# Performance work log

Measured on AMD Instinct MI355X. Metric: run time of the kernel, lower is better.

Reference implementation:

```python
import jax, jax.numpy as jnp
import numpy as np

EMB = 512
HEADS = 8
HEAD_DIM = EMB // HEADS


def setup_inputs() -> dict:
    key = jax.random.key(0)
    ks = jax.random.split(key, 9)
    s = 1.0 / np.sqrt(EMB)
    return {
        "x": jax.random.normal(ks[0], (4, 2048, EMB), dtype=jnp.float32),
        "Wq": jax.random.uniform(ks[1], (EMB, EMB), jnp.float32, -s, s),
        "bq": jax.random.uniform(ks[2], (EMB,), jnp.float32, -s, s),
        "Wk": jax.random.uniform(ks[3], (EMB, EMB), jnp.float32, -s, s),
        "bk": jax.random.uniform(ks[4], (EMB,), jnp.float32, -s, s),
        "Wv": jax.random.uniform(ks[5], (EMB, EMB), jnp.float32, -s, s),
        "bv": jax.random.uniform(ks[6], (EMB,), jnp.float32, -s, s),
        "Wp": jax.random.uniform(ks[7], (EMB, EMB), jnp.float32, -s, s),
        "bp": jax.random.uniform(ks[8], (EMB,), jnp.float32, -s, s),
    }


def _split_heads(t):
    b, n, _ = t.shape
    return t.reshape(b, n, HEADS, HEAD_DIM).transpose(0, 2, 1, 3)  # b h n d


def reference(x, Wq, bq, Wk, bk, Wv, bv, Wp, bp):
    q = _split_heads(x @ Wq.T + bq)
    k = _split_heads(x @ Wk.T + bk)
    v = _split_heads(x @ Wv.T + bv)
    energy = jnp.einsum("bhqd,bhkd->bhqk", q, k)
    # NOTE: original applies softmax to UNSCALED logits, then divides probs by sqrt(emb)
    att = jax.nn.softmax(energy, axis=-1) / jnp.sqrt(jnp.float32(EMB))
    out = jnp.einsum("bhqk,bhkd->bhqd", att, v)
    b, h, n, d = out.shape
    out = out.transpose(0, 2, 1, 3).reshape(b, n, h * d)
    return out @ Wp.T + bp
```

## Files before the change

kernel.cpp:

```cpp
#include <hip/hip_runtime.h>
#include <math.h>
#include <stdint.h>

#define SEQ  2048
#define NH   8
#define HD   64
#define MTOT 8192
#define LOG2E 1.4426950408889634f

typedef __attribute__((ext_vector_type(4))) float f32x4;
typedef __attribute__((ext_vector_type(8))) short bf16x8;

__device__ __forceinline__ unsigned short bfu(float f) {
    return (unsigned short)((__float_as_uint(f) + 0x8000u) >> 16);
}
__device__ __forceinline__ unsigned packbf(float a, float b) {
    return __builtin_amdgcn_perm(__float_as_uint(b) + 0x8000u,
                                 __float_as_uint(a) + 0x8000u, 0x07060302u);
}

__device__ __forceinline__ void gl_lds16(const void* g, const void* l) {
    __builtin_amdgcn_global_load_lds(
        (const __attribute__((address_space(1))) unsigned int*)g,
        (__attribute__((address_space(3))) unsigned int*)l, 16, 0, 0);
}

__global__ __launch_bounds__(256) void convert_kernel(
    const float* __restrict__ x,  const float* __restrict__ wq,
    const float* __restrict__ wk, const float* __restrict__ wv,
    const float* __restrict__ wp, unsigned short* __restrict__ dst)
{
    const long i = ((long)blockIdx.x * 256 + threadIdx.x) * 4;
    if (i >= 5242880L) return;
    const float* src; long off;
    if      (i < 4194304L) { src = x;  off = i; }
    else if (i < 4456448L) { src = wq; off = i - 4194304L; }
    else if (i < 4718592L) { src = wk; off = i - 4456448L; }
    else if (i < 4980736L) { src = wv; off = i - 4718592L; }
    else                   { src = wp; off = i - 4980736L; }
    const float4 a = *(const float4*)(src + off);
    uint2 o;
    o.x = packbf(a.x, a.y);
    o.y = packbf(a.z, a.w);
    *(uint2*)(dst + i) = o;
}

template <int MODE>
__global__ __launch_bounds__(256, 2) void gemm_kernel(
    const unsigned short* __restrict__ A, const unsigned short* __restrict__ W,
    const float* __restrict__ b0, const float* __restrict__ b1,
    const float* __restrict__ b2,
    unsigned short* __restrict__ Qw, unsigned short* __restrict__ Kw,
    unsigned short* __restrict__ VTw, float* __restrict__ Fout)
{
    constexpr int BN = (MODE == 0) ? 128 : 64;
    constexpr int NT = BN / 32;
    constexpr int BSTR = BN * 32;
    __shared__ __align__(16) unsigned short smem[16384];
    const int t = threadIdx.x;
    const int w = t >> 6, lane = t & 63, quad = (t >> 4) & 3, l15 = t & 15;
    const int wr = w >> 1, wc = w & 1;
    const int m0 = blockIdx.y * 128, n0 = blockIdx.x * BN;

    f32x4 acc[4][NT];
#pragma unroll
    for (int mt = 0; mt < 4; ++mt)
#pragma unroll
        for (int nt = 0; nt < NT; ++nt) acc[mt][nt] = (f32x4){0.f, 0.f, 0.f, 0.f};

    auto stage = [&](int buf, int k0) {
#pragma unroll
        for (int i = 0; i < 2; ++i) {
            const int ci = w * 2 + i;
            gl_lds16(A + (size_t)(m0 + ci * 16 + l15) * 512 + k0 + quad * 8,
                     smem + buf * 4096 + ci * 512);
            if (MODE == 0)
                gl_lds16(W + (size_t)(n0 + ci * 16 + l15) * 512 + k0 + quad * 8,
                         smem + 8192 + buf * BSTR + ci * 512);
        }
        if (MODE == 1)
            gl_lds16(W + (size_t)(n0 + w * 16 + l15) * 512 + k0 + quad * 8,
                     smem + 8192 + buf * BSTR + w * 512);
    };

    stage(0, 0);
    __syncthreads();
    int buf = 0;
    for (int ki = 0; ki < 16; ++ki) {
        if (ki < 15) stage(buf ^ 1, (ki + 1) * 32);
        const unsigned short* As = smem + buf * 4096;
        const unsigned short* Bs = smem + 8192 + buf * BSTR;
        bf16x8 af[4], bfr[NT];
#pragma unroll
        for (int mt = 0; mt < 4; ++mt)
            af[mt] = *(const bf16x8*)(As + ((wr * 4 + mt) * 64 + lane) * 8);
#pragma unroll
        for (int nt = 0; nt < NT; ++nt)
            bfr[nt] = *(const bf16x8*)(Bs + ((wc * NT + nt) * 64 + lane) * 8);
#pragma unroll
        for (int mt = 0; mt < 4; ++mt)
#pragma unroll
            for (int nt = 0; nt < NT; ++nt)
                acc[mt][nt] = __builtin_amdgcn_mfma_f32_16x16x32_bf16(
                    af[mt], bfr[nt], acc[mt][nt], 0, 0, 0);
        buf ^= 1;
        if (ki < 15) __syncthreads();
    }

#pragma unroll
    for (int nt = 0; nt < NT; ++nt) {
        const int n = n0 + wc * (BN / 2) + nt * 16 + l15;
        float bias, sc = 1.f;
        int which = 0;
        if (MODE == 0) {
            which = n >> 9;
            const float* bp = which == 0 ? b0 : (which == 1 ? b1 : b2);
            bias = bp[n & 511];
            if (which == 0) sc = LOG2E;
        } else {
            bias = b0[n];
        }
#pragma unroll
        for (int mt = 0; mt < 4; ++mt) {
            const int mb = m0 + wr * 64 + mt * 16 + quad * 4;
            const f32x4 v = acc[mt][nt];
            if (MODE == 1) {
#pragma unroll
                for (int r = 0; r < 4; ++r)
                    Fout[(size_t)(mb + r) * 512 + n] = v[r] + bias;
            } else {
                const int bi = mb >> 11, ns = mb & 2047;
                const int h = (n >> 6) & 7, d = n & 63;
                if (which < 2) {
                    unsigned short* dst =
                        (which ? Kw : Qw) + ((size_t)(bi * 8 + h) * SEQ + ns) * 64 + d;
#pragma unroll
                    for (int r = 0; r < 4; ++r) dst[r * 64] = bfu((v[r] + bias) * sc);
                } else {
                    unsigned short* dst =
                        VTw + ((size_t)(bi * 8 + h) * 64 + d) * SEQ + ns;
                    uint2 pk;
                    pk.x = packbf(v[0] + bias, v[1] + bias);
                    pk.y = packbf(v[2] + bias, v[3] + bias);
                    *(uint2*)dst = pk;
                }
            }
        }
    }
}

__global__ __launch_bounds__(256, 2) void attn_kernel(
    const unsigned short* __restrict__ Q, const unsigned short* __restrict__ K,
    const unsigned short* __restrict__ VT, unsigned short* __restrict__ Ow)
{
    __shared__ __align__(16) unsigned short smem[24576];
    const int t = threadIdx.x;
    const int w = t >> 6, lane = t & 63, quad = (t >> 4) & 3, l15 = t & 15;

    const int bh = blockIdx.x;
    const int q0 = blockIdx.y * 128;

    const unsigned short* Qb = Q + ((size_t)bh * SEQ + q0) * 64;
    const unsigned short* Kb = K + (size_t)bh * SEQ * 64;
    const unsigned short* Vb = VT + (size_t)bh * 64 * SEQ;

#pragma unroll
    for (int i = 0; i < 4; ++i) {
        const int ci = w * 4 + i, g = ci >> 1, hf = ci & 1;
        gl_lds16(Qb + (size_t)(g * 16 + l15) * 64 + hf * 32 + quad * 8,
                 smem + ci * 512);
    }

    auto stageKV = [&](int buf, int j0) {
#pragma unroll
        for (int i = 0; i < 2; ++i) {
            const int ci = w * 2 + i, jg = ci >> 1, hf = ci & 1;
            gl_lds16(Kb + (size_t)(j0 + jg * 16 + l15) * 64 + hf * 32 + quad * 8,
                     smem + 8192 + buf * 4096 + ci * 512);
            gl_lds16(Vb + (size_t)(jg * 16 + l15) * SEQ + j0 + hf * 32 + quad * 8,
                     smem + 16384 + buf * 4096 + ci * 512);
        }
    };

    stageKV(0, 0);
    __syncthreads();

    bf16x8 qf[2][2];
#pragma unroll
    for (int g = 0; g < 2; ++g)
#pragma unroll
        for (int h = 0; h < 2; ++h)
            qf[g][h] = *(const bf16x8*)(smem + (((w * 2 + g) * 2 + h) * 512) + lane * 8);

    float lpart[2] = {0.f, 0.f};
    f32x4 O[2][4];
#pragma unroll
    for (int g = 0; g < 2; ++g)
#pragma unroll
        for (int dt = 0; dt < 4; ++dt) O[g][dt] = (f32x4){0.f, 0.f, 0.f, 0.f};

    const int srcA = (quad & 1) * 32 + l15;
    const int srcB = srcA + 16;
    const bool hi = (quad >> 1) != 0;

    int buf = 0;
    for (int jt = 0; jt < 32; ++jt) {
        if (jt < 31) stageKV(buf ^ 1, (jt + 1) * 64);
        const unsigned short* Ks = smem + 8192 + buf * 4096;
        const unsigned short* Vs = smem + 16384 + buf * 4096;

        f32x4 s[2][4];
        const f32x4 z = {0.f, 0.f, 0.f, 0.f};
#pragma unroll
        for (int mt = 0; mt < 4; ++mt) {
            const bf16x8 k0 = *(const bf16x8*)(Ks + ((mt * 2 + 0) * 64 + lane) * 8);
            const bf16x8 k1 = *(const bf16x8*)(Ks + ((mt * 2 + 1) * 64 + lane) * 8);
#pragma unroll
            for (int g = 0; g < 2; ++g) {
                s[g][mt] = __builtin_amdgcn_mfma_f32_16x16x32_bf16(k0, qf[g][0], z, 0, 0, 0);
                s[g][mt] = __builtin_amdgcn_mfma_f32_16x16x32_bf16(k1, qf[g][1], s[g][mt], 0, 0, 0);
            }
        }

        unsigned pk[2][4][2];
#pragma unroll
        for (int g = 0; g < 2; ++g) {
            float lp = 0.f;
#pragma unroll
            for (int mt = 0; mt < 4; ++mt) {
                const float e0 = __builtin_amdgcn_exp2f(s[g][mt][0]);
                const float e1 = __builtin_amdgcn_exp2f(s[g][mt][1]);
                const float e2 = __builtin_amdgcn_exp2f(s[g][mt][2]);
                const float e3 = __builtin_amdgcn_exp2f(s[g][mt][3]);
                lp += (e0 + e1) + (e2 + e3);
                pk[g][mt][0] = packbf(e0, e1);
                pk[g][mt][1] = packbf(e2, e3);
            }
            lpart[g] += lp;
        }

#pragma unroll
        for (int kt = 0; kt < 2; ++kt) {
            bf16x8 pu[2];
#pragma unroll
            for (int g = 0; g < 2; ++g) {
                unsigned t0, t1;
                union { unsigned u[4]; bf16x8 v; } pb;
                t0 = (unsigned)__shfl((int)pk[g][2 * kt][0], srcA);
                t1 = (unsigned)__shfl((int)pk[g][2 * kt + 1][0], srcA);
                pb.u[0] = hi ? t1 : t0;
                t0 = (unsigned)__shfl((int)pk[g][2 * kt][1], srcA);
                t1 = (unsigned)__shfl((int)pk[g][2 * kt + 1][1], srcA);
                pb.u[1] = hi ? t1 : t0;
                t0 = (unsigned)__shfl((int)pk[g][2 * kt][0], srcB);
                t1 = (unsigned)__shfl((int)pk[g][2 * kt + 1][0], srcB);
                pb.u[2] = hi ? t1 : t0;
                t0 = (unsigned)__shfl((int)pk[g][2 * kt][1], srcB);
                t1 = (unsigned)__shfl((int)pk[g][2 * kt + 1][1], srcB);
                pb.u[3] = hi ? t1 : t0;
                pu[g] = pb.v;
            }
#pragma unroll
            for (int dt = 0; dt < 4; ++dt) {
                const bf16x8 vf =
                    *(const bf16x8*)(Vs + ((dt * 2 + kt) * 64 + lane) * 8);
#pragma unroll
                for (int g = 0; g < 2; ++g)
                    O[g][dt] = __builtin_amdgcn_mfma_f32_16x16x32_bf16(
                        vf, pu[g], O[g][dt], 0, 0, 0);
            }
        }

        buf ^= 1;
        if (jt < 31) __syncthreads();
    }

    const int bi = bh >> 3, h = bh & 7;
#pragma unroll
    for (int g = 0; g < 2; ++g) {
        float lv = lpart[g];
        lv += __shfl_xor(lv, 16);
        lv += __shfl_xor(lv, 32);
        const float inv = 1.0f / (lv * 22.627416997969522f);
        const int ns = q0 + (w * 2 + g) * 16 + l15;
        unsigned short* dst0 = Ow + ((size_t)bi * SEQ + ns) * 512 + h * 64 + quad * 4;
#pragma unroll
        for (int dt = 0; dt < 4; ++dt) {
            uint2 pkv;
            pkv.x = packbf(O[g][dt][0] * inv, O[g][dt][1] * inv);
            pkv.y = packbf(O[g][dt][2] * inv, O[g][dt][3] * inv);
            *(uint2*)(dst0 + dt * 16) = pkv;
        }
    }
}

extern "C" void kernel_launch(void* const* d_in, const int* in_sizes, int n_in,
                              void* d_out, int out_size, void* d_ws, size_t ws_size,
                              hipStream_t stream)
{
    const float* x  = (const float*)d_in[0];
    const float* Wq = (const float*)d_in[1];
    const float* bq = (const float*)d_in[2];
    const float* Wk = (const float*)d_in[3];
    const float* bk = (const float*)d_in[4];
    const float* Wv = (const float*)d_in[5];
    const float* bv = (const float*)d_in[6];
    const float* Wp = (const float*)d_in[7];
    const float* bp = (const float*)d_in[8];

    unsigned short* ws = (unsigned short*)d_ws;
    unsigned short* xb    = ws;
    unsigned short* Wqkvb = ws + 4194304;
    unsigned short* Wpb   = ws + 4980736;
    unsigned short* Qw    = ws + 5242880;
    unsigned short* Kw    = Qw + 4194304;
    unsigned short* VTw   = Kw + 4194304;
    unsigned short* Owb   = VTw + 4194304;

    convert_kernel<<<5120, 256, 0, stream>>>(x, Wq, Wk, Wv, Wp, ws);
    gemm_kernel<0><<<dim3(12, 64), 256, 0, stream>>>(
        xb, Wqkvb, bq, bk, bv, Qw, Kw, VTw, nullptr);
    attn_kernel<<<dim3(32, 16), 256, 0, stream>>>(Qw, Kw, VTw, Owb);
    gemm_kernel<1><<<dim3(8, 64), 256, 0, stream>>>(
        Owb, Wpb, bp, nullptr, nullptr, nullptr, nullptr, nullptr, (float*)d_out);
}
```

Before: 186.1 us.

## Use 32x32x16 MFMA in attention and split QKV GEMM with transposed Q/K epilogue

The attention kernel moves from 16x16x32 MFMA tiles to 32x32x16 tiles, with each wave owning 32 query rows. This changes the LDS staging layout for Q, K and V and replaces the multi-shuffle P relayout with a single xor-32 exchange. The QKV projection is split into two launches. Q/K use a transposed MFMA operand order so each lane writes 4 contiguous bf16 values instead of scattered 2-byte stores, and V keeps the original VT epilogue. The risks are a second kernel launch and higher accumulator register pressure from the f32x16 tiles.

```diff
diff --git a/kernel.cpp b/kernel.cpp
--- a/kernel.cpp
+++ b/kernel.cpp
@@ -9,6 +9,7 @@
 #define LOG2E 1.4426950408889634f
 
 typedef __attribute__((ext_vector_type(4))) float f32x4;
+typedef __attribute__((ext_vector_type(16))) float f32x16;
 typedef __attribute__((ext_vector_type(8))) short bf16x8;
 
 __device__ __forceinline__ unsigned short bfu(float f) {
@@ -45,7 +46,7 @@
     *(uint2*)(dst + i) = o;
 }
 
-template <int MODE>
+template <int MODE, int TR>
 __global__ __launch_bounds__(256, 2) void gemm_kernel(
     const unsigned short* __restrict__ A, const unsigned short* __restrict__ W,
     const float* __restrict__ b0, const float* __restrict__ b1,
@@ -60,7 +61,8 @@
     const int t = threadIdx.x;
     const int w = t >> 6, lane = t & 63, quad = (t >> 4) & 3, l15 = t & 15;
     const int wr = w >> 1, wc = w & 1;
-    const int m0 = blockIdx.y * 128, n0 = blockIdx.x * BN;
+    const int m0 = blockIdx.y * 128;
+    const int n0 = blockIdx.x * BN + ((MODE == 0 && TR == 0) ? 1024 : 0);
 
     f32x4 acc[4][NT];
 #pragma unroll
@@ -100,50 +102,72 @@
 #pragma unroll
         for (int mt = 0; mt < 4; ++mt)
 #pragma unroll
-            for (int nt = 0; nt < NT; ++nt)
-                acc[mt][nt] = __builtin_amdgcn_mfma_f32_16x16x32_bf16(
-                    af[mt], bfr[nt], acc[mt][nt], 0, 0, 0);
+            for (int nt = 0; nt < NT; ++nt) {
+                if (TR)
+                    acc[mt][nt] = __builtin_amdgcn_mfma_f32_16x16x32_bf16(
+                        bfr[nt], af[mt], acc[mt][nt], 0, 0, 0);
+                else
+                    acc[mt][nt] = __builtin_amdgcn_mfma_f32_16x16x32_bf16(
+                        af[mt], bfr[nt], acc[mt][nt], 0, 0, 0);
+            }
         buf ^= 1;
         if (ki < 15) __syncthreads();
     }
 
-#pragma unroll
-    for (int nt = 0; nt < NT; ++nt) {
-        const int n = n0 + wc * (BN / 2) + nt * 16 + l15;
-        float bias, sc = 1.f;
-        int which = 0;
-        if (MODE == 0) {
-            which = n >> 9;
-            const float* bp = which == 0 ? b0 : (which == 1 ? b1 : b2);
-            bias = bp[n & 511];
-            if (which == 0) sc = LOG2E;
-        } else {
-            bias = b0[n];
-        }
-#pragma unroll
-        for (int mt = 0; mt < 4; ++mt) {
-            const int mb = m0 + wr * 64 + mt * 16 + quad * 4;
-            const f32x4 v = acc[mt][nt];
-            if (MODE == 1) {
+    if (MODE == 1) {
+#pragma unroll
+        for (int nt = 0; nt < NT; ++nt) {
+            const int n = n0 + wc * 32 + nt * 16 + l15;
+            const float bias = b0[n];
+#pragma unroll
+            for (int mt = 0; mt < 4; ++mt) {
+                const int mb = m0 + wr * 64 + mt * 16 + quad * 4;
+                const f32x4 v = acc[mt][nt];
 #pragma unroll
                 for (int r = 0; r < 4; ++r)
                     Fout[(size_t)(mb + r) * 512 + n] = v[r] + bias;
-            } else {
+            }
+        }
+    } else if (TR == 0) {
+#pragma unroll
+        for (int nt = 0; nt < 4; ++nt) {
+            const int n = n0 + wc * 64 + nt * 16 + l15;
+            const float bias = b2[n & 511];
+            const int h = (n >> 6) & 7, d = n & 63;
+#pragma unroll
+            for (int mt = 0; mt < 4; ++mt) {
+                const int mb = m0 + wr * 64 + mt * 16 + quad * 4;
                 const int bi = mb >> 11, ns = mb & 2047;
-                const int h = (n >> 6) & 7, d = n & 63;
-                if (which < 2) {
-                    unsigned short* dst =
-                        (which ? Kw : Qw) + ((size_t)(bi * 8 + h) * SEQ + ns) * 64 + d;
-#pragma unroll
-                    for (int r = 0; r < 4; ++r) dst[r * 64] = bfu((v[r] + bias) * sc);
-                } else {
-                    unsigned short* dst =
-                        VTw + ((size_t)(bi * 8 + h) * 64 + d) * SEQ + ns;
-                    uint2 pk;
-                    pk.x = packbf(v[0] + bias, v[1] + bias);
-                    pk.y = packbf(v[2] + bias, v[3] + bias);
-                    *(uint2*)dst = pk;
-                }
+                const f32x4 v = acc[mt][nt];
+                unsigned short* dst =
+                    VTw + ((size_t)(bi * 8 + h) * 64 + d) * SEQ + ns;
+                uint2 pk;
+                pk.x = packbf(v[0] + bias, v[1] + bias);
+                pk.y = packbf(v[2] + bias, v[3] + bias);
+                *(uint2*)dst = pk;
+            }
+        }
+    } else {
+        const int which = n0 >> 9;
+        const float sc = which ? 1.f : LOG2E;
+        const float* bp = which ? b1 : b0;
+        unsigned short* base = which ? Kw : Qw;
+#pragma unroll
+        for (int nt = 0; nt < 4; ++nt) {
+            const int nb = n0 + wc * 64 + nt * 16 + quad * 4;
+            const f32x4 bv = *(const f32x4*)(bp + (nb & 511));
+            const int h = (nb >> 6) & 7, d0 = nb & 63;
+#pragma unroll
+            for (int mt = 0; mt < 4; ++mt) {
+                const int nsg = m0 + wr * 64 + mt * 16 + l15;
+                const int bi = nsg >> 11, ns = nsg & 2047;
+                const f32x4 v = acc[mt][nt];
+                const float f0 = (v[0] + bv[0]) * sc, f1 = (v[1] + bv[1]) * sc;
+                const float f2 = (v[2] + bv[2]) * sc, f3 = (v[3] + bv[3]) * sc;
+                uint2 pk;
+                pk.x = packbf(f0, f1);
+                pk.y = packbf(f2, f3);
+                *(uint2*)(base + ((size_t)(bi * 8 + h) * SEQ + ns) * 64 + d0) = pk;
             }
         }
     }
@@ -155,7 +179,8 @@
 {
     __shared__ __align__(16) unsigned short smem[24576];
     const int t = threadIdx.x;
-    const int w = t >> 6, lane = t & 63, quad = (t >> 4) & 3, l15 = t & 15;
+    const int w = t >> 6, lane = t & 63;
+    const int l31 = lane & 31, hlf = lane >> 5;
 
     const int bh = blockIdx.x;
     const int q0 = blockIdx.y * 128;
@@ -165,43 +190,37 @@
     const unsigned short* Vb = VT + (size_t)bh * 64 * SEQ;
 
 #pragma unroll
-    for (int i = 0; i < 4; ++i) {
-        const int ci = w * 4 + i, g = ci >> 1, hf = ci & 1;
-        gl_lds16(Qb + (size_t)(g * 16 + l15) * 64 + hf * 32 + quad * 8,
-                 smem + ci * 512);
-    }
+    for (int i = 0; i < 4; ++i)
+        gl_lds16(Qb + (size_t)(w * 32 + l31) * 64 + i * 16 + hlf * 8,
+                 smem + (w * 4 + i) * 512);
 
     auto stageKV = [&](int buf, int j0) {
 #pragma unroll
         for (int i = 0; i < 2; ++i) {
-            const int ci = w * 2 + i, jg = ci >> 1, hf = ci & 1;
-            gl_lds16(Kb + (size_t)(j0 + jg * 16 + l15) * 64 + hf * 32 + quad * 8,
-                     smem + 8192 + buf * 4096 + ci * 512);
-            gl_lds16(Vb + (size_t)(jg * 16 + l15) * SEQ + j0 + hf * 32 + quad * 8,
-                     smem + 16384 + buf * 4096 + ci * 512);
+            const int c = w * 2 + i;
+            const int g = c >> 2, s = c & 3;
+            gl_lds16(Kb + (size_t)(j0 + g * 32 + l31) * 64 + s * 16 + hlf * 8,
+                     smem + 8192 + buf * 4096 + c * 512);
+            gl_lds16(Vb + (size_t)(g * 32 + l31) * SEQ + j0 + s * 16 + hlf * 8,
+                     smem + 16384 + buf * 4096 + c * 512);
         }
     };
 
     stageKV(0, 0);
     __syncthreads();
 
-    bf16x8 qf[2][2];
-#pragma unroll
-    for (int g = 0; g < 2; ++g)
-#pragma unroll
-        for (int h = 0; h < 2; ++h)
-            qf[g][h] = *(const bf16x8*)(smem + (((w * 2 + g) * 2 + h) * 512) + lane * 8);
-
-    float lpart[2] = {0.f, 0.f};
-    f32x4 O[2][4];
-#pragma unroll
-    for (int g = 0; g < 2; ++g)
-#pragma unroll
-        for (int dt = 0; dt < 4; ++dt) O[g][dt] = (f32x4){0.f, 0.f, 0.f, 0.f};
-
-    const int srcA = (quad & 1) * 32 + l15;
-    const int srcB = srcA + 16;
-    const bool hi = (quad >> 1) != 0;
+    bf16x8 qf[4];
+#pragma unroll
+    for (int i = 0; i < 4; ++i)
+        qf[i] = *(const bf16x8*)(smem + (w * 4 + i) * 512 + lane * 8);
+
+    f32x16 zero;
+#pragma unroll
+    for (int r = 0; r < 16; ++r) zero[r] = 0.f;
+
+    float lpart = 0.f;
+    f32x16 Ot[2];
+    Ot[0] = zero; Ot[1] = zero;
 
     int buf = 0;
     for (int jt = 0; jt < 32; ++jt) {
@@ -209,89 +228,79 @@
         const unsigned short* Ks = smem + 8192 + buf * 4096;
         const unsigned short* Vs = smem + 16384 + buf * 4096;
 
-        f32x4 s[2][4];
-        const f32x4 z = {0.f, 0.f, 0.f, 0.f};
-#pragma unroll
-        for (int mt = 0; mt < 4; ++mt) {
-            const bf16x8 k0 = *(const bf16x8*)(Ks + ((mt * 2 + 0) * 64 + lane) * 8);
-            const bf16x8 k1 = *(const bf16x8*)(Ks + ((mt * 2 + 1) * 64 + lane) * 8);
-#pragma unroll
-            for (int g = 0; g < 2; ++g) {
-                s[g][mt] = __builtin_amdgcn_mfma_f32_16x16x32_bf16(k0, qf[g][0], z, 0, 0, 0);
-                s[g][mt] = __builtin_amdgcn_mfma_f32_16x16x32_bf16(k1, qf[g][1], s[g][mt], 0, 0, 0);
-            }
-        }
-
-        unsigned pk[2][4][2];
-#pragma unroll
-        for (int g = 0; g < 2; ++g) {
-            float lp = 0.f;
-#pragma unroll
-            for (int mt = 0; mt < 4; ++mt) {
-                const float e0 = __builtin_amdgcn_exp2f(s[g][mt][0]);
-                const float e1 = __builtin_amdgcn_exp2f(s[g][mt][1]);
-                const float e2 = __builtin_amdgcn_exp2f(s[g][mt][2]);
-                const float e3 = __builtin_amdgcn_exp2f(s[g][mt][3]);
-                lp += (e0 + e1) + (e2 + e3);
-                pk[g][mt][0] = packbf(e0, e1);
-                pk[g][mt][1] = packbf(e2, e3);
-            }
-            lpart[g] += lp;
-        }
-
-#pragma unroll
-        for (int kt = 0; kt < 2; ++kt) {
-            bf16x8 pu[2];
-#pragma unroll
-            for (int g = 0; g < 2; ++g) {
-                unsigned t0, t1;
-                union { unsigned u[4]; bf16x8 v; } pb;
-                t0 = (unsigned)__shfl((int)pk[g][2 * kt][0], srcA);
-                t1 = (unsigned)__shfl((int)pk[g][2 * kt + 1][0], srcA);
-                pb.u[0] = hi ? t1 : t0;
-                t0 = (unsigned)__shfl((int)pk[g][2 * kt][1], srcA);
-                t1 = (unsigned)__shfl((int)pk[g][2 * kt + 1][1], srcA);
-                pb.u[1] = hi ? t1 : t0;
-                t0 = (unsigned)__shfl((int)pk[g][2 * kt][0], srcB);
-                t1 = (unsigned)__shfl((int)pk[g][2 * kt + 1][0], srcB);
-                pb.u[2] = hi ? t1 : t0;
-                t0 = (unsigned)__shfl((int)pk[g][2 * kt][1], srcB);
-                t1 = (unsigned)__shfl((int)pk[g][2 * kt + 1][1], srcB);
-                pb.u[3] = hi ? t1 : t0;
-                pu[g] = pb.v;
-            }
-#pragma unroll
-            for (int dt = 0; dt < 4; ++dt) {
+        f32x16 st[2];
+#pragma unroll
+        for (int jg = 0; jg < 2; ++jg) {
+            f32x16 c = zero;
+#pragma unroll
+            for (int kt = 0; kt < 4; ++kt) {
+                const bf16x8 kf =
+                    *(const bf16x8*)(Ks + (jg * 4 + kt) * 512 + lane * 8);
+                c = __builtin_amdgcn_mfma_f32_32x32x16_bf16(kf, qf[kt], c, 0, 0, 0);
+            }
+            st[jg] = c;
+        }
+
+        float ls = 0.f;
+#pragma unroll
+        for (int jg = 0; jg < 2; ++jg)
+#pragma unroll
+            for (int r = 0; r < 16; ++r) {
+                st[jg][r] = __builtin_amdgcn_exp2f(st[jg][r]);
+                ls += st[jg][r];
+            }
+        lpart += ls;
+
+        bf16x8 pf[4];
+#pragma unroll
+        for (int p = 0; p < 4; ++p) {
+            const f32x16 c = st[p >> 1];
+            const int r0 = (p & 1) * 8;
+            const unsigned a0 = packbf(c[r0 + 0], c[r0 + 1]);
+            const unsigned a1 = packbf(c[r0 + 2], c[r0 + 3]);
+            const unsigned b0 = packbf(c[r0 + 4], c[r0 + 5]);
+            const unsigned b1 = packbf(c[r0 + 6], c[r0 + 7]);
+            const unsigned ta0 = (unsigned)__shfl_xor((int)a0, 32);
+            const unsigned ta1 = (unsigned)__shfl_xor((int)a1, 32);
+            const unsigned tb0 = (unsigned)__shfl_xor((int)b0, 32);
+            const unsigned tb1 = (unsigned)__shfl_xor((int)b1, 32);
+            union { unsigned u[4]; bf16x8 v; } pb;
+            pb.u[0] = hlf ? tb0 : a0;
+            pb.u[1] = hlf ? tb1 : a1;
+            pb.u[2] = hlf ? b0 : ta0;
+            pb.u[3] = hlf ? b1 : ta1;
+            pf[p] = pb.v;
+        }
+
+#pragma unroll
+        for (int dg = 0; dg < 2; ++dg)
+#pragma unroll
+            for (int p = 0; p < 4; ++p) {
                 const bf16x8 vf =
-                    *(const bf16x8*)(Vs + ((dt * 2 + kt) * 64 + lane) * 8);
-#pragma unroll
-                for (int g = 0; g < 2; ++g)
-                    O[g][dt] = __builtin_amdgcn_mfma_f32_16x16x32_bf16(
-                        vf, pu[g], O[g][dt], 0, 0, 0);
-            }
-        }
+                    *(const bf16x8*)(Vs + (dg * 4 + p) * 512 + lane * 8);
+                Ot[dg] = __builtin_amdgcn_mfma_f32_32x32x16_bf16(
+                    vf, pf[p], Ot[dg], 0, 0, 0);
+            }
 
         buf ^= 1;
         if (jt < 31) __syncthreads();
     }
 
+    const float lv = lpart + __shfl_xor(lpart, 32);
+    const float inv = 1.0f / (lv * 22.627416997969522f);
+
     const int bi = bh >> 3, h = bh & 7;
-#pragma unroll
-    for (int g = 0; g < 2; ++g) {
-        float lv = lpart[g];
-        lv += __shfl_xor(lv, 16);
-        lv += __shfl_xor(lv, 32);
-        const float inv = 1.0f / (lv * 22.627416997969522f);
-        const int ns = q0 + (w * 2 + g) * 16 + l15;
-        unsigned short* dst0 = Ow + ((size_t)bi * SEQ + ns) * 512 + h * 64 + quad * 4;
-#pragma unroll
-        for (int dt = 0; dt < 4; ++dt) {
-            uint2 pkv;
-            pkv.x = packbf(O[g][dt][0] * inv, O[g][dt][1] * inv);
-            pkv.y = packbf(O[g][dt][2] * inv, O[g][dt][3] * inv);
-            *(uint2*)(dst0 + dt * 16) = pkv;
-        }
-    }
+    const int ns = q0 + w * 32 + l31;
+    unsigned short* dst = Ow + ((size_t)bi * SEQ + ns) * 512 + h * 64 + hlf * 4;
+#pragma unroll
+    for (int dg = 0; dg < 2; ++dg)
+#pragma unroll
+        for (int rb = 0; rb < 4; ++rb) {
+            uint2 pk;
+            pk.x = packbf(Ot[dg][rb * 4 + 0] * inv, Ot[dg][rb * 4 + 1] * inv);
+            pk.y = packbf(Ot[dg][rb * 4 + 2] * inv, Ot[dg][rb * 4 + 3] * inv);
+            *(uint2*)(dst + dg * 32 + rb * 8) = pk;
+        }
 }
 
 extern "C" void kernel_launch(void* const* d_in, const int* in_sizes, int n_in,
@@ -318,9 +327,11 @@
     unsigned short* Owb   = VTw + 4194304;
 
     convert_kernel<<<5120, 256, 0, stream>>>(x, Wq, Wk, Wv, Wp, ws);
-    gemm_kernel<0><<<dim3(12, 64), 256, 0, stream>>>(
+    gemm_kernel<0, 1><<<dim3(8, 64), 256, 0, stream>>>(
+        xb, Wqkvb, bq, bk, bv, Qw, Kw, VTw, nullptr);
+    gemm_kernel<0, 0><<<dim3(4, 64), 256, 0, stream>>>(
         xb, Wqkvb, bq, bk, bv, Qw, Kw, VTw, nullptr);
     attn_kernel<<<dim3(32, 16), 256, 0, stream>>>(Qw, Kw, VTw, Owb);
-    gemm_kernel<1><<<dim3(8, 64), 256, 0, stream>>>(
+    gemm_kernel<1, 0><<<dim3(8, 64), 256, 0, stream>>>(
         Owb, Wpb, bp, nullptr, nullptr, nullptr, nullptr, nullptr, (float*)d_out);
 }
```

Result: no change. 184.8 us (-0.7%).
